# Optimization experiments

Hardware: AMD Instinct MI355X
Metric: run time of the kernel (lower is better)

The kernel has to match this reference:

```python
import jax, jax.numpy as jnp
import numpy as np

EPS_RMS = 1.1920929e-07  # torch F.rms_norm default eps = finfo(float32).eps
N_EMBD = 64
N_QKV = 256


def _silu(t):
    return t * jax.nn.sigmoid(t)


def _rms_norm(t):
    return t * jax.lax.rsqrt(jnp.mean(t * t, axis=-1, keepdims=True) + EPS_RMS)


def _w_norm(w, n):
    target_std = n ** (-0.5)
    return w * (target_std / (jnp.std(w, ddof=1) + 1e-08))


def setup_inputs() -> dict:
    key = jax.random.key(0)
    ks = jax.random.split(key, 7)
    B, T = 8, 8192
    x = jax.random.normal(ks[0], (B, T, N_EMBD), dtype=jnp.float32)
    y = jax.random.normal(ks[1], (B, T, N_QKV), dtype=jnp.float32)
    # CastedLinear init: uniform(-s, s), s = sqrt(3)/sqrt(in_features)
    def lin(k, out_f, in_f):
        s = (3.0 ** 0.5) * in_f ** (-0.5)
        return jax.random.uniform(k, (out_f, in_f), jnp.float32, -s, s)
    w_qkv = lin(ks[2], 3 * N_QKV, N_EMBD)          # [768, 64]
    w_swiglu = lin(ks[3], 2 * N_EMBD, N_QKV)       # [128, 256]
    w_out = lin(ks[4], N_EMBD, N_EMBD)             # [64, 64]
    out_w = lin(ks[5], N_EMBD, N_EMBD)             # self.out weight [64, 64]
    tao = lin(ks[6], 3, 1)                          # [3, 1]
    return {"x": x, "y": y, "w_qkv": w_qkv, "w_swiglu": w_swiglu,
            "w_out": w_out, "out_w": out_w, "tao": tao}


def reference(x, y, w_qkv, w_swiglu, w_out, out_w, tao):
    B = x.shape[0]
    # SwiGLU branch: F.linear(y, w_swiglu) -> [B,T,2*n_embd], chunk
    uv = jnp.einsum('btq,eq->bte', y, w_swiglu)
    u, v = jnp.split(uv, 2, axis=-1)                 # each [B,T,64]
    y_out = x + jnp.einsum('btd,ed->bte', u * _silu(v), w_out)

    # gates
    g = jnp.clip(jnp.abs(tao), 1e-08, 1.0)           # [3,1]
    alpha, beta, gamma = g[0], g[1], g[2]

    # Hebbian outer-product memory: mean_b(u^T v) * n_embd^-0.5, rms-normed
    ao = jnp.einsum('btd,bte->de', u, v) / B * (N_EMBD ** (-0.5))  # [64,64]
    ao = _rms_norm(ao)

    # update w_qkv
    n1 = _silu(w_qkv @ ao)                            # [768,64]
    w_qkv_new = _w_norm(w_qkv + n1 @ out_w.T, N_EMBD) * alpha

    # update w_swiglu: view(64, 512).T @ ao
    n2 = _silu(w_swiglu.reshape(N_EMBD, 2 * N_QKV).T @ ao)  # [512,64]
    n2 = n2 @ out_w.T                                  # [512,64]
    w_swiglu_new = w_swiglu + n2.T.reshape(2 * N_EMBD, N_QKV)
    w_swiglu_new = _w_norm(w_swiglu_new, N_QKV) * beta

    # update w_out
    n3 = _silu(w_out @ ao)                             # [64,64]
    w_out_new = _w_norm(w_out + n3 @ out_w.T, N_QKV) * gamma

    return (y_out, w_qkv_new, w_swiglu_new, w_out_new)
```

## Files before the change

### kernel.cpp

```cpp
#include <hip/hip_runtime.h>
#include <cstdint>

typedef short short8 __attribute__((ext_vector_type(8)));
typedef float floatx4 __attribute__((ext_vector_type(4)));

#define MFMA_BF16 __builtin_amdgcn_mfma_f32_16x16x32_bf16

__device__ __forceinline__ short f2bf(float f) {
  union { float f; unsigned u; } a; a.f = f;
  unsigned r = a.u + 0x7FFFu + ((a.u >> 16) & 1u);
  return (short)(r >> 16);
}

__device__ __forceinline__ float silu_f(float v) {
  return v / (1.0f + __expf(-v));
}

#define QDIM 256
#define DEMB 64
#define TILE_T 32
#define ITERS 4
#define NBLK1 512
#define YSTR 264
#define UVSTR 132
#define HSTR 72

#define OFF_QKV 4194304
#define OFF_SW  4243456
#define OFF_WO  4276224

#define AO_COPIES 8
#define WS_SUMS   32768
#define WS_AOT    32776

__global__ __launch_bounds__(256, 2) void k1_main(
    const float* __restrict__ x, const float* __restrict__ y,
    const float* __restrict__ w_sw, const float* __restrict__ w_out,
    float* __restrict__ y_out, float* __restrict__ ao_copies)
{
  __shared__ __align__(16) short Ylds[TILE_T * YSTR];
  __shared__ __align__(16) float UVlds[TILE_T * UVSTR];
  __shared__ __align__(16) short Hlds[TILE_T * HSTR];

  const int tid  = threadIdx.x;
  const int lane = tid & 63;
  const int wave = tid >> 6;
  const int l15  = lane & 15;
  const int quad = lane >> 4;
  const floatx4 fzero = {0.f, 0.f, 0.f, 0.f};

  short8 b1[2][8];
#pragma unroll
  for (int nt = 0; nt < 2; ++nt) {
    const float* wr = w_sw + (size_t)(wave * 32 + nt * 16 + l15) * QDIM;
#pragma unroll
    for (int kt = 0; kt < 8; ++kt) {
      const float* p = wr + kt * 32 + quad * 8;
      short8 f;
#pragma unroll
      for (int j = 0; j < 8; ++j) f[j] = f2bf(p[j]);
      b1[nt][kt] = f;
    }
  }
  short8 b2[2];
  {
    const float* wr = w_out + (size_t)(wave * 16 + l15) * DEMB;
#pragma unroll
    for (int kt = 0; kt < 2; ++kt) {
      const float* p = wr + kt * 32 + quad * 8;
      short8 f;
#pragma unroll
      for (int j = 0; j < 8; ++j) f[j] = f2bf(p[j]);
      b2[kt] = f;
    }
  }

  floatx4 ao_acc[4];
#pragma unroll
  for (int i = 0; i < 4; ++i) ao_acc[i] = fzero;

  const int tok0 = blockIdx.x * (TILE_T * ITERS);

  for (int it = 0; it < ITERS; ++it) {
    const int tbase = tok0 + it * TILE_T;

    {
      const float4* src = (const float4*)(y + (size_t)tbase * QDIM);
#pragma unroll
      for (int rep = 0; rep < 8; ++rep) {
        int i = tid + rep * 256;
        float4 f = src[i];
        int tok = i >> 6;
        int col = (i & 63) * 4;
        short* dst = &Ylds[tok * YSTR + col];
        dst[0] = f2bf(f.x); dst[1] = f2bf(f.y);
        dst[2] = f2bf(f.z); dst[3] = f2bf(f.w);
      }
    }
    __syncthreads();

    floatx4 acc[2][2];
#pragma unroll
    for (int a = 0; a < 2; ++a)
#pragma unroll
      for (int b = 0; b < 2; ++b) acc[a][b] = fzero;
#pragma unroll
    for (int kt = 0; kt < 8; ++kt) {
      short8 a0 = *(const short8*)&Ylds[(l15)      * YSTR + kt * 32 + quad * 8];
      short8 a1 = *(const short8*)&Ylds[(16 + l15) * YSTR + kt * 32 + quad * 8];
      acc[0][0] = MFMA_BF16(a0, b1[0][kt], acc[0][0], 0, 0, 0);
      acc[0][1] = MFMA_BF16(a0, b1[1][kt], acc[0][1], 0, 0, 0);
      acc[1][0] = MFMA_BF16(a1, b1[0][kt], acc[1][0], 0, 0, 0);
      acc[1][1] = MFMA_BF16(a1, b1[1][kt], acc[1][1], 0, 0, 0);
    }
#pragma unroll
    for (int mt = 0; mt < 2; ++mt)
#pragma unroll
      for (int nt = 0; nt < 2; ++nt)
#pragma unroll
        for (int r = 0; r < 4; ++r)
          UVlds[(mt * 16 + quad * 4 + r) * UVSTR + wave * 32 + nt * 16 + l15] =
              acc[mt][nt][r];
    __syncthreads();

    {
      int t = tid >> 3;
      int d0 = (tid & 7) * 8;
      const float* uvrow = &UVlds[t * UVSTR];
      short8 pack;
#pragma unroll
      for (int j = 0; j < 8; ++j) {
        float u = uvrow[d0 + j];
        float v = uvrow[64 + d0 + j];
        pack[j] = f2bf(u * silu_f(v));
      }
      *(short8*)&Hlds[t * HSTR + d0] = pack;
    }

    {
      short8 a3;
#pragma unroll
      for (int j = 0; j < 8; ++j)
        a3[j] = f2bf(UVlds[(quad * 8 + j) * UVSTR + wave * 16 + l15]);
#pragma unroll
      for (int et = 0; et < 4; ++et) {
        short8 b3;
#pragma unroll
        for (int j = 0; j < 8; ++j)
          b3[j] = f2bf(UVlds[(quad * 8 + j) * UVSTR + 64 + et * 16 + l15]);
        ao_acc[et] = MFMA_BF16(a3, b3, ao_acc[et], 0, 0, 0);
      }
    }
    __syncthreads();

#pragma unroll
    for (int mt = 0; mt < 2; ++mt) {
      floatx4 acc2 = fzero;
#pragma unroll
      for (int kt = 0; kt < 2; ++kt) {
        short8 a2 = *(const short8*)&Hlds[(mt * 16 + l15) * HSTR + kt * 32 + quad * 8];
        acc2 = MFMA_BF16(a2, b2[kt], acc2, 0, 0, 0);
      }
      int e = wave * 16 + l15;
#pragma unroll
      for (int r = 0; r < 4; ++r) {
        size_t idx = (size_t)(tbase + mt * 16 + quad * 4 + r) * DEMB + e;
        y_out[idx] = x[idx] + acc2[r];
      }
    }
    __syncthreads();
  }

  float* dst = ao_copies + (blockIdx.x & (AO_COPIES - 1)) * 4096;
#pragma unroll
  for (int et = 0; et < 4; ++et)
#pragma unroll
    for (int r = 0; r < 4; ++r) {
      int d = wave * 16 + quad * 4 + r;
      int e = et * 16 + l15;
      atomicAdd(&dst[d * 64 + e], ao_acc[et][r]);
    }
}

__global__ __launch_bounds__(256) void k2_finalize(
    const float* __restrict__ ao_copies, unsigned short* __restrict__ aoT)
{
  __shared__ float aoFT[64 * 65];
  __shared__ float ssPart[256];
  __shared__ float scRow[64];
  const int tid = threadIdx.x;

#pragma unroll
  for (int k = 0; k < 16; ++k) {
    int idx = k * 256 + tid;
    float v = 0.f;
#pragma unroll
    for (int c = 0; c < AO_COPIES; ++c) v += ao_copies[c * 4096 + idx];
    v *= (1.0f / 64.0f);
    int d = idx >> 6, e = idx & 63;
    aoFT[e * 65 + d] = v;
  }
  __syncthreads();

  {
    int d = tid >> 2, q = tid & 3;
    float ssp = 0.f;
#pragma unroll
    for (int e2 = 0; e2 < 16; ++e2) {
      float v = aoFT[(q * 16 + e2) * 65 + d];
      ssp += v * v;
    }
    ssPart[tid] = ssp;
  }
  __syncthreads();
  if (tid < 64) {
    float ss = ssPart[tid * 4] + ssPart[tid * 4 + 1] +
               ssPart[tid * 4 + 2] + ssPart[tid * 4 + 3];
    scRow[tid] = rsqrtf(ss * (1.0f / 64.0f) + 1.1920929e-07f);
  }
  __syncthreads();

#pragma unroll
  for (int k = 0; k < 16; ++k) {
    int j = k * 256 + tid;
    int e = j >> 6, d = j & 63;
    float v = aoFT[e * 65 + d] * scRow[d];
    aoT[j] = (unsigned short)f2bf(v);
  }
}

__global__ __launch_bounds__(64) void k3_updates(
    const float* __restrict__ w_qkv, const float* __restrict__ w_sw,
    const float* __restrict__ w_out, const float* __restrict__ out_w,
    const unsigned short* __restrict__ aoT, float* __restrict__ out,
    float* __restrict__ sums)
{
  __shared__ __align__(16) short Nlds[16 * 72];
  const int lane = threadIdx.x;
  const int l15  = lane & 15;
  const int quad = lane >> 4;
  const int rid  = blockIdx.x;
  const floatx4 fzero = {0.f, 0.f, 0.f, 0.f};
  const short8* aoTv = (const short8*)aoT;

  short8 bf[2][4];
#pragma unroll
  for (int kt = 0; kt < 2; ++kt)
#pragma unroll
    for (int nt = 0; nt < 4; ++nt)
      bf[kt][nt] = aoTv[(nt * 16 + l15) * 8 + kt * 4 + quad];

  short8 af[2];
  if (rid < 48) {
    const float* wr = w_qkv + (size_t)(rid * 16 + l15) * 64;
#pragma unroll
    for (int kt = 0; kt < 2; ++kt) {
      const float* p = wr + kt * 32 + quad * 8;
      short8 f;
#pragma unroll
      for (int j = 0; j < 8; ++j) f[j] = f2bf(p[j]);
      af[kt] = f;
    }
  } else if (rid < 80) {
    int p0 = (rid - 48) * 16;
#pragma unroll
    for (int kt = 0; kt < 2; ++kt) {
      short8 f;
#pragma unroll
      for (int j = 0; j < 8; ++j) {
        int a = kt * 32 + quad * 8 + j;
        f[j] = f2bf(w_sw[a * 512 + p0 + l15]);
      }
      af[kt] = f;
    }
  } else {
    const float* wr = w_out + (size_t)((rid - 80) * 16 + l15) * 64;
#pragma unroll
    for (int kt = 0; kt < 2; ++kt) {
      const float* p = wr + kt * 32 + quad * 8;
      short8 f;
#pragma unroll
      for (int j = 0; j < 8; ++j) f[j] = f2bf(p[j]);
      af[kt] = f;
    }
  }

  floatx4 acc[4];
#pragma unroll
  for (int nt = 0; nt < 4; ++nt) acc[nt] = fzero;
#pragma unroll
  for (int kt = 0; kt < 2; ++kt)
#pragma unroll
    for (int nt = 0; nt < 4; ++nt)
      acc[nt] = MFMA_BF16(af[kt], bf[kt][nt], acc[nt], 0, 0, 0);
#pragma unroll
  for (int nt = 0; nt < 4; ++nt)
#pragma unroll
    for (int r = 0; r < 4; ++r)
      Nlds[(quad * 4 + r) * 72 + nt * 16 + l15] = f2bf(silu_f(acc[nt][r]));
  __syncthreads();

  float s1 = 0.f, s2 = 0.f;
  int matrix;

  if (rid < 48 || rid >= 80) {
    matrix = (rid < 48) ? 0 : 2;
    short8 a2[2];
#pragma unroll
    for (int kt = 0; kt < 2; ++kt)
      a2[kt] = *(const short8*)&Nlds[l15 * 72 + kt * 32 + quad * 8];
    short8 b2[2][4];
#pragma unroll
    for (int nt = 0; nt < 4; ++nt) {
      const float* wr = out_w + (size_t)(nt * 16 + l15) * 64;
#pragma unroll
      for (int kt = 0; kt < 2; ++kt) {
        const float* p = wr + kt * 32 + quad * 8;
        short8 f;
#pragma unroll
        for (int j = 0; j < 8; ++j) f[j] = f2bf(p[j]);
        b2[kt][nt] = f;
      }
    }
    floatx4 acc2[4];
#pragma unroll
    for (int nt = 0; nt < 4; ++nt) acc2[nt] = fzero;
#pragma unroll
    for (int kt = 0; kt < 2; ++kt)
#pragma unroll
      for (int nt = 0; nt < 4; ++nt)
        acc2[nt] = MFMA_BF16(a2[kt], b2[kt][nt], acc2[nt], 0, 0, 0);

    const float* Wsrc = (rid < 48) ? w_qkv : w_out;
    int base_row = (rid < 48) ? rid * 16 : (rid - 80) * 16;
    int off      = (rid < 48) ? OFF_QKV : OFF_WO;
#pragma unroll
    for (int nt = 0; nt < 4; ++nt)
#pragma unroll
      for (int r = 0; r < 4; ++r) {
        int row = base_row + quad * 4 + r;
        int col = nt * 16 + l15;
        float val = Wsrc[row * 64 + col] + acc2[nt][r];
        out[off + row * 64 + col] = val;
        s1 += val; s2 += val * val;
      }
  } else {
    matrix = 1;
    int p0 = (rid - 48) * 16;
    short8 b2[2];
#pragma unroll
    for (int kt = 0; kt < 2; ++kt)
      b2[kt] = *(const short8*)&Nlds[l15 * 72 + kt * 32 + quad * 8];
    short8 a2[4][2];
#pragma unroll
    for (int mt = 0; mt < 4; ++mt) {
      const float* wr = out_w + (size_t)(mt * 16 + l15) * 64;
#pragma unroll
      for (int kt = 0; kt < 2; ++kt) {
        const float* p = wr + kt * 32 + quad * 8;
        short8 f;
#pragma unroll
        for (int j = 0; j < 8; ++j) f[j] = f2bf(p[j]);
        a2[mt][kt] = f;
      }
    }
    floatx4 acc2[4];
#pragma unroll
    for (int mt = 0; mt < 4; ++mt) acc2[mt] = fzero;
#pragma unroll
    for (int mt = 0; mt < 4; ++mt)
#pragma unroll
      for (int kt = 0; kt < 2; ++kt)
        acc2[mt] = MFMA_BF16(a2[mt][kt], b2[kt], acc2[mt], 0, 0, 0);
#pragma unroll
    for (int mt = 0; mt < 4; ++mt)
#pragma unroll
      for (int r = 0; r < 4; ++r) {
        int a = mt * 16 + quad * 4 + r;
        int p = p0 + l15;
        int idx = a * 512 + p;
        float val = w_sw[idx] + acc2[mt][r];
        out[OFF_SW + idx] = val;
        s1 += val; s2 += val * val;
      }
  }

#pragma unroll
  for (int off = 32; off > 0; off >>= 1) {
    s1 += __shfl_down(s1, off);
    s2 += __shfl_down(s2, off);
  }
  if (lane == 0) {
    atomicAdd(&sums[matrix * 2],     s1);
    atomicAdd(&sums[matrix * 2 + 1], s2);
  }
}

__global__ __launch_bounds__(256) void k4_scale(
    float* __restrict__ out, const float* __restrict__ sums,
    const float* __restrict__ tao)
{
  int i = blockIdx.x * 256 + threadIdx.x;
  int matrix, idx; float N, tstd;
  if (i < 49152)      { matrix = 0; idx = OFF_QKV + i;           N = 49152.f; tstd = 0.125f;  }
  else if (i < 81920) { matrix = 1; idx = OFF_SW + (i - 49152);  N = 32768.f; tstd = 0.0625f; }
  else                { matrix = 2; idx = OFF_WO + (i - 81920);  N = 4096.f;  tstd = 0.0625f; }
  float sum = sums[matrix * 2], sumsq = sums[matrix * 2 + 1];
  float mean = sum / N;
  float var  = (sumsq - N * mean * mean) / (N - 1.f);
  float sd   = sqrtf(fmaxf(var, 0.f));
  float g    = fminf(fmaxf(fabsf(tao[matrix]), 1e-8f), 1.0f);
  out[idx] *= g * tstd / (sd + 1e-8f);
}

extern "C" void kernel_launch(void* const* d_in, const int* in_sizes, int n_in,
                              void* d_out, int out_size, void* d_ws, size_t ws_size,
                              hipStream_t stream) {
  const float* x     = (const float*)d_in[0];
  const float* y     = (const float*)d_in[1];
  const float* w_qkv = (const float*)d_in[2];
  const float* w_sw  = (const float*)d_in[3];
  const float* w_out = (const float*)d_in[4];
  const float* out_w = (const float*)d_in[5];
  const float* tao   = (const float*)d_in[6];
  float* out = (float*)d_out;
  float* ws  = (float*)d_ws;

  float* ao_copies    = ws;
  float* sums         = ws + WS_SUMS;
  unsigned short* aoT = (unsigned short*)(ws + WS_AOT);

  hipMemsetAsync(d_ws, 0, (WS_SUMS + 8) * sizeof(float), stream);
  k1_main<<<dim3(NBLK1), dim3(256), 0, stream>>>(x, y, w_sw, w_out, out, ao_copies);
  k2_finalize<<<dim3(1), dim3(256), 0, stream>>>(ao_copies, aoT);
  k3_updates<<<dim3(84), dim3(64), 0, stream>>>(w_qkv, w_sw, w_out, out_w,
                                                aoT, out, sums);
  k4_scale<<<dim3(336), dim3(256), 0, stream>>>(out, sums, tao);
}
```

Baseline: 145.6 us.

## Fuse ao finalize into main kernel via last-block counter and prefetch y

```diff
diff --git a/kernel.cpp b/kernel.cpp
--- a/kernel.cpp
+++ b/kernel.cpp
@@ -2,6 +2,7 @@
 #include <cstdint>
 
 typedef short short8 __attribute__((ext_vector_type(8)));
+typedef short short4_t __attribute__((ext_vector_type(4)));
 typedef float floatx4 __attribute__((ext_vector_type(4)));
 
 #define MFMA_BF16 __builtin_amdgcn_mfma_f32_16x16x32_bf16
@@ -11,7 +12,11 @@
   unsigned r = a.u + 0x7FFFu + ((a.u >> 16) & 1u);
   return (short)(r >> 16);
 }
-
+__device__ __forceinline__ float bf2f(short s) {
+  union { unsigned u; float f; } a;
+  a.u = ((unsigned)(unsigned short)s) << 16;
+  return a.f;
+}
 __device__ __forceinline__ float silu_f(float v) {
   return v / (1.0f + __expf(-v));
 }
@@ -22,7 +27,7 @@
 #define ITERS 4
 #define NBLK1 512
 #define YSTR 264
-#define UVSTR 132
+#define TSTR 40
 #define HSTR 72
 
 #define OFF_QKV 4194304
@@ -33,14 +38,24 @@
 #define WS_SUMS   32768
 #define WS_AOT    32776
 
+#define SM_Y   0
+#define SM_UVT 16896
+#define SM_H   27136
+#define SM_TOT 31744
+#define SM_AOFT 0
+#define SM_SSP  16640
+#define SM_SCR  17664
+
 __global__ __launch_bounds__(256, 2) void k1_main(
     const float* __restrict__ x, const float* __restrict__ y,
     const float* __restrict__ w_sw, const float* __restrict__ w_out,
-    float* __restrict__ y_out, float* __restrict__ ao_copies)
+    float* __restrict__ y_out, float* __restrict__ ao_copies,
+    unsigned int* __restrict__ counter, unsigned short* __restrict__ aoT)
 {
-  __shared__ __align__(16) short Ylds[TILE_T * YSTR];
-  __shared__ __align__(16) float UVlds[TILE_T * UVSTR];
-  __shared__ __align__(16) short Hlds[TILE_T * HSTR];
+  __shared__ __align__(16) char smem[SM_TOT];
+  short* Ylds = (short*)(smem + SM_Y);
+  short* UVT  = (short*)(smem + SM_UVT);
+  short* Hlds = (short*)(smem + SM_H);
 
   const int tid  = threadIdx.x;
   const int lane = tid & 63;
@@ -48,6 +63,14 @@
   const int l15  = lane & 15;
   const int quad = lane >> 4;
   const floatx4 fzero = {0.f, 0.f, 0.f, 0.f};
+  const int tok0 = blockIdx.x * (TILE_T * ITERS);
+
+  float4 yreg[8];
+  {
+    const float4* src = (const float4*)(y + (size_t)tok0 * QDIM);
+#pragma unroll
+    for (int rep = 0; rep < 8; ++rep) yreg[rep] = src[tid + rep * 256];
+  }
 
   short8 b1[2][8];
 #pragma unroll
@@ -79,23 +102,33 @@
 #pragma unroll
   for (int i = 0; i < 4; ++i) ao_acc[i] = fzero;
 
-  const int tok0 = blockIdx.x * (TILE_T * ITERS);
+  float xreg[8];
 
   for (int it = 0; it < ITERS; ++it) {
     const int tbase = tok0 + it * TILE_T;
 
+#pragma unroll
+    for (int rep = 0; rep < 8; ++rep) {
+      int i = tid + rep * 256;
+      int tok = i >> 6;
+      int col = (i & 63) * 4;
+      float4 f = yreg[rep];
+      short4_t p4 = { f2bf(f.x), f2bf(f.y), f2bf(f.z), f2bf(f.w) };
+      *(short4_t*)&Ylds[tok * YSTR + col] = p4;
+    }
+
+    if (it + 1 < ITERS) {
+      const float4* src = (const float4*)(y + (size_t)(tbase + TILE_T) * QDIM);
+#pragma unroll
+      for (int rep = 0; rep < 8; ++rep) yreg[rep] = src[tid + rep * 256];
+    }
     {
-      const float4* src = (const float4*)(y + (size_t)tbase * QDIM);
-#pragma unroll
-      for (int rep = 0; rep < 8; ++rep) {
-        int i = tid + rep * 256;
-        float4 f = src[i];
-        int tok = i >> 6;
-        int col = (i & 63) * 4;
-        short* dst = &Ylds[tok * YSTR + col];
-        dst[0] = f2bf(f.x); dst[1] = f2bf(f.y);
-        dst[2] = f2bf(f.z); dst[3] = f2bf(f.w);
-      }
+      const float* xb = x + (size_t)tbase * DEMB + wave * 16 + l15;
+#pragma unroll
+      for (int mt = 0; mt < 2; ++mt)
+#pragma unroll
+        for (int r = 0; r < 4; ++r)
+          xreg[mt * 4 + r] = xb[(mt * 16 + quad * 4 + r) * DEMB];
     }
     __syncthreads();
 
@@ -116,38 +149,32 @@
 #pragma unroll
     for (int mt = 0; mt < 2; ++mt)
 #pragma unroll
-      for (int nt = 0; nt < 2; ++nt)
-#pragma unroll
-        for (int r = 0; r < 4; ++r)
-          UVlds[(mt * 16 + quad * 4 + r) * UVSTR + wave * 32 + nt * 16 + l15] =
-              acc[mt][nt][r];
+      for (int nt = 0; nt < 2; ++nt) {
+        short4_t p4;
+#pragma unroll
+        for (int r = 0; r < 4; ++r) p4[r] = f2bf(acc[mt][nt][r]);
+        int c  = wave * 32 + nt * 16 + l15;
+        int t0 = mt * 16 + quad * 4;
+        *(short4_t*)&UVT[c * TSTR + t0] = p4;
+      }
     __syncthreads();
 
     {
-      int t = tid >> 3;
-      int d0 = (tid & 7) * 8;
-      const float* uvrow = &UVlds[t * UVSTR];
-      short8 pack;
+      int d  = tid & 63;
+      int t0 = (tid >> 6) * 8;
+      short8 u8 = *(const short8*)&UVT[d * TSTR + t0];
+      short8 v8 = *(const short8*)&UVT[(64 + d) * TSTR + t0];
 #pragma unroll
       for (int j = 0; j < 8; ++j) {
-        float u = uvrow[d0 + j];
-        float v = uvrow[64 + d0 + j];
-        pack[j] = f2bf(u * silu_f(v));
-      }
-      *(short8*)&Hlds[t * HSTR + d0] = pack;
-    }
-
+        float h = bf2f(u8[j]) * silu_f(bf2f(v8[j]));
+        Hlds[(t0 + j) * HSTR + d] = f2bf(h);
+      }
+    }
     {
-      short8 a3;
-#pragma unroll
-      for (int j = 0; j < 8; ++j)
-        a3[j] = f2bf(UVlds[(quad * 8 + j) * UVSTR + wave * 16 + l15]);
+      short8 a3 = *(const short8*)&UVT[(wave * 16 + l15) * TSTR + quad * 8];
 #pragma unroll
       for (int et = 0; et < 4; ++et) {
-        short8 b3;
-#pragma unroll
-        for (int j = 0; j < 8; ++j)
-          b3[j] = f2bf(UVlds[(quad * 8 + j) * UVSTR + 64 + et * 16 + l15]);
+        short8 b3 = *(const short8*)&UVT[(64 + et * 16 + l15) * TSTR + quad * 8];
         ao_acc[et] = MFMA_BF16(a3, b3, ao_acc[et], 0, 0, 0);
       }
     }
@@ -165,10 +192,9 @@
 #pragma unroll
       for (int r = 0; r < 4; ++r) {
         size_t idx = (size_t)(tbase + mt * 16 + quad * 4 + r) * DEMB + e;
-        y_out[idx] = x[idx] + acc2[r];
-      }
-    }
-    __syncthreads();
+        y_out[idx] = xreg[mt * 4 + r] + acc2[r];
+      }
+    }
   }
 
   float* dst = ao_copies + (blockIdx.x & (AO_COPIES - 1)) * 4096;
@@ -180,15 +206,18 @@
       int e = et * 16 + l15;
       atomicAdd(&dst[d * 64 + e], ao_acc[et][r]);
     }
-}
-
-__global__ __launch_bounds__(256) void k2_finalize(
-    const float* __restrict__ ao_copies, unsigned short* __restrict__ aoT)
-{
-  __shared__ float aoFT[64 * 65];
-  __shared__ float ssPart[256];
-  __shared__ float scRow[64];
-  const int tid = threadIdx.x;
+
+  __threadfence();
+  __syncthreads();
+  __shared__ int lastFlag;
+  if (tid == 0) lastFlag = (atomicAdd(counter, 1u) == NBLK1 - 1) ? 1 : 0;
+  __syncthreads();
+  if (!lastFlag) return;
+  __threadfence();
+
+  float* aoFT = (float*)(smem + SM_AOFT);
+  float* ssP  = (float*)(smem + SM_SSP);
+  float* scR  = (float*)(smem + SM_SCR);
 
 #pragma unroll
   for (int k = 0; k < 16; ++k) {
@@ -201,7 +230,6 @@
     aoFT[e * 65 + d] = v;
   }
   __syncthreads();
-
   {
     int d = tid >> 2, q = tid & 3;
     float ssp = 0.f;
@@ -210,22 +238,19 @@
       float v = aoFT[(q * 16 + e2) * 65 + d];
       ssp += v * v;
     }
-    ssPart[tid] = ssp;
+    ssP[tid] = ssp;
   }
   __syncthreads();
   if (tid < 64) {
-    float ss = ssPart[tid * 4] + ssPart[tid * 4 + 1] +
-               ssPart[tid * 4 + 2] + ssPart[tid * 4 + 3];
-    scRow[tid] = rsqrtf(ss * (1.0f / 64.0f) + 1.1920929e-07f);
-  }
-  __syncthreads();
-
+    float ss = ssP[tid * 4] + ssP[tid * 4 + 1] + ssP[tid * 4 + 2] + ssP[tid * 4 + 3];
+    scR[tid] = rsqrtf(ss * (1.0f / 64.0f) + 1.1920929e-07f);
+  }
+  __syncthreads();
 #pragma unroll
   for (int k = 0; k < 16; ++k) {
     int j = k * 256 + tid;
     int e = j >> 6, d = j & 63;
-    float v = aoFT[e * 65 + d] * scRow[d];
-    aoT[j] = (unsigned short)f2bf(v);
+    aoT[j] = (unsigned short)f2bf(aoFT[e * 65 + d] * scR[d]);
   }
 }
 
@@ -426,13 +451,14 @@
   float* out = (float*)d_out;
   float* ws  = (float*)d_ws;
 
-  float* ao_copies    = ws;
-  float* sums         = ws + WS_SUMS;
-  unsigned short* aoT = (unsigned short*)(ws + WS_AOT);
+  float* ao_copies      = ws;
+  float* sums           = ws + WS_SUMS;
+  unsigned int* counter = (unsigned int*)(ws + WS_SUMS + 6);
+  unsigned short* aoT   = (unsigned short*)(ws + WS_AOT);
 
   hipMemsetAsync(d_ws, 0, (WS_SUMS + 8) * sizeof(float), stream);
-  k1_main<<<dim3(NBLK1), dim3(256), 0, stream>>>(x, y, w_sw, w_out, out, ao_copies);
-  k2_finalize<<<dim3(1), dim3(256), 0, stream>>>(ao_copies, aoT);
+  k1_main<<<dim3(NBLK1), dim3(256), 0, stream>>>(x, y, w_sw, w_out, out,
+                                                 ao_copies, counter, aoT);
   k3_updates<<<dim3(84), dim3(64), 0, stream>>>(w_qkv, w_sw, w_out, out_w,
                                                 aoT, out, sums);
   k4_scale<<<dim3(336), dim3(256), 0, stream>>>(out, sums, tao);
```

Result: slower. 217.3 us (+49.2%).

## Stage UV tile as transposed bf16 in LDS and halve per-block token count

Applied to the files above, without the earlier changes.

```diff
diff --git a/kernel.cpp b/kernel.cpp
--- a/kernel.cpp
+++ b/kernel.cpp
@@ -2,6 +2,7 @@
 #include <cstdint>
 
 typedef short short8 __attribute__((ext_vector_type(8)));
+typedef short short4_t __attribute__((ext_vector_type(4)));
 typedef float floatx4 __attribute__((ext_vector_type(4)));
 
 #define MFMA_BF16 __builtin_amdgcn_mfma_f32_16x16x32_bf16
@@ -11,7 +12,11 @@
   unsigned r = a.u + 0x7FFFu + ((a.u >> 16) & 1u);
   return (short)(r >> 16);
 }
-
+__device__ __forceinline__ float bf2f(short s) {
+  union { unsigned u; float f; } a;
+  a.u = ((unsigned)(unsigned short)s) << 16;
+  return a.f;
+}
 __device__ __forceinline__ float silu_f(float v) {
   return v / (1.0f + __expf(-v));
 }
@@ -19,19 +24,19 @@
 #define QDIM 256
 #define DEMB 64
 #define TILE_T 32
-#define ITERS 4
-#define NBLK1 512
+#define ITERS 2
+#define NBLK1 1024
 #define YSTR 264
-#define UVSTR 132
+#define TSTR 40
 #define HSTR 72
 
 #define OFF_QKV 4194304
 #define OFF_SW  4243456
 #define OFF_WO  4276224
 
-#define AO_COPIES 8
-#define WS_SUMS   32768
-#define WS_AOT    32776
+#define AO_COPIES 16
+#define WS_SUMS   65536
+#define WS_AOT    65544
 
 __global__ __launch_bounds__(256, 2) void k1_main(
     const float* __restrict__ x, const float* __restrict__ y,
@@ -39,7 +44,7 @@
     float* __restrict__ y_out, float* __restrict__ ao_copies)
 {
   __shared__ __align__(16) short Ylds[TILE_T * YSTR];
-  __shared__ __align__(16) float UVlds[TILE_T * UVSTR];
+  __shared__ __align__(16) short UVT[128 * TSTR];
   __shared__ __align__(16) short Hlds[TILE_T * HSTR];
 
   const int tid  = threadIdx.x;
@@ -48,6 +53,7 @@
   const int l15  = lane & 15;
   const int quad = lane >> 4;
   const floatx4 fzero = {0.f, 0.f, 0.f, 0.f};
+  const int tok0 = blockIdx.x * (TILE_T * ITERS);
 
   short8 b1[2][8];
 #pragma unroll
@@ -78,8 +84,6 @@
   floatx4 ao_acc[4];
 #pragma unroll
   for (int i = 0; i < 4; ++i) ao_acc[i] = fzero;
-
-  const int tok0 = blockIdx.x * (TILE_T * ITERS);
 
   for (int it = 0; it < ITERS; ++it) {
     const int tbase = tok0 + it * TILE_T;
@@ -92,9 +96,8 @@
         float4 f = src[i];
         int tok = i >> 6;
         int col = (i & 63) * 4;
-        short* dst = &Ylds[tok * YSTR + col];
-        dst[0] = f2bf(f.x); dst[1] = f2bf(f.y);
-        dst[2] = f2bf(f.z); dst[3] = f2bf(f.w);
+        short4_t p4 = { f2bf(f.x), f2bf(f.y), f2bf(f.z), f2bf(f.w) };
+        *(short4_t*)&Ylds[tok * YSTR + col] = p4;
       }
     }
     __syncthreads();
@@ -116,38 +119,32 @@
 #pragma unroll
     for (int mt = 0; mt < 2; ++mt)
 #pragma unroll
-      for (int nt = 0; nt < 2; ++nt)
-#pragma unroll
-        for (int r = 0; r < 4; ++r)
-          UVlds[(mt * 16 + quad * 4 + r) * UVSTR + wave * 32 + nt * 16 + l15] =
-              acc[mt][nt][r];
+      for (int nt = 0; nt < 2; ++nt) {
+        short4_t p4;
+#pragma unroll
+        for (int r = 0; r < 4; ++r) p4[r] = f2bf(acc[mt][nt][r]);
+        int c  = wave * 32 + nt * 16 + l15;
+        int t0 = mt * 16 + quad * 4;
+        *(short4_t*)&UVT[c * TSTR + t0] = p4;
+      }
     __syncthreads();
 
     {
-      int t = tid >> 3;
-      int d0 = (tid & 7) * 8;
-      const float* uvrow = &UVlds[t * UVSTR];
-      short8 pack;
+      int d  = tid & 63;
+      int t0 = (tid >> 6) * 8;
+      short8 u8 = *(const short8*)&UVT[d * TSTR + t0];
+      short8 v8 = *(const short8*)&UVT[(64 + d) * TSTR + t0];
 #pragma unroll
       for (int j = 0; j < 8; ++j) {
-        float u = uvrow[d0 + j];
-        float v = uvrow[64 + d0 + j];
-        pack[j] = f2bf(u * silu_f(v));
-      }
-      *(short8*)&Hlds[t * HSTR + d0] = pack;
-    }
-
+        float h = bf2f(u8[j]) * silu_f(bf2f(v8[j]));
+        Hlds[(t0 + j) * HSTR + d] = f2bf(h);
+      }
+    }
     {
-      short8 a3;
-#pragma unroll
-      for (int j = 0; j < 8; ++j)
-        a3[j] = f2bf(UVlds[(quad * 8 + j) * UVSTR + wave * 16 + l15]);
+      short8 a3 = *(const short8*)&UVT[(wave * 16 + l15) * TSTR + quad * 8];
 #pragma unroll
       for (int et = 0; et < 4; ++et) {
-        short8 b3;
-#pragma unroll
-        for (int j = 0; j < 8; ++j)
-          b3[j] = f2bf(UVlds[(quad * 8 + j) * UVSTR + 64 + et * 16 + l15]);
+        short8 b3 = *(const short8*)&UVT[(64 + et * 16 + l15) * TSTR + quad * 8];
         ao_acc[et] = MFMA_BF16(a3, b3, ao_acc[et], 0, 0, 0);
       }
     }
@@ -168,7 +165,6 @@
         y_out[idx] = x[idx] + acc2[r];
       }
     }
-    __syncthreads();
   }
 
   float* dst = ao_copies + (blockIdx.x & (AO_COPIES - 1)) * 4096;
@@ -201,7 +197,6 @@
     aoFT[e * 65 + d] = v;
   }
   __syncthreads();
-
   {
     int d = tid >> 2, q = tid & 3;
     float ssp = 0.f;
@@ -219,13 +214,11 @@
     scRow[tid] = rsqrtf(ss * (1.0f / 64.0f) + 1.1920929e-07f);
   }
   __syncthreads();
-
 #pragma unroll
   for (int k = 0; k < 16; ++k) {
     int j = k * 256 + tid;
     int e = j >> 6, d = j & 63;
-    float v = aoFT[e * 65 + d] * scRow[d];
-    aoT[j] = (unsigned short)f2bf(v);
+    aoT[j] = (unsigned short)f2bf(aoFT[e * 65 + d] * scRow[d]);
   }
 }
 
```

After: 155.1 us. 1.07x slower.
